# Optimization experiments

Hardware: AMD Instinct MI355X
Metric: run time of the kernel (lower is better)

## Reference

```python
import jax, jax.numpy as jnp
import numpy as np
from jax import lax

D_MODEL = 1024
D_STATE = 16
EXPAND = 2
KERNEL = 4
BATCH = 4
SEQ = 4096
LN_EPS = 1e-5


def _ln(x, w, b):
    m = jnp.mean(x, axis=-1, keepdims=True)
    v = jnp.mean((x - m) ** 2, axis=-1, keepdims=True)
    return (x - m) * lax.rsqrt(v + LN_EPS) * w + b


def setup_inputs() -> dict:
    key = jax.random.key(0)
    ks = jax.random.split(key, 16)
    d, n, e, k = D_MODEL, D_STATE, EXPAND, KERNEL

    def lin(key, fan_in, shape):
        bound = 1.0 / np.sqrt(fan_in)
        return jax.random.uniform(key, shape, jnp.float32, -bound, bound)

    return {
        "x": jax.random.normal(ks[0], (BATCH, SEQ, d), jnp.float32),
        "ln1_w": jnp.ones((d,), jnp.float32),
        "ln1_b": jnp.zeros((d,), jnp.float32),
        "conv_w": lin(ks[1], k, (d, 1, k)),  # depthwise conv, groups=d -> fan_in=k
        "conv_b": lin(ks[2], k, (d,)),
        "lns_w": jnp.ones((d,), jnp.float32),
        "lns_b": jnp.zeros((d,), jnp.float32),
        "in_w": lin(ks[3], d, (d, 2 * d)),
        "in_b": lin(ks[4], d, (2 * d,)),
        "xp_w": lin(ks[5], d, (d, n)),
        "xp_b": lin(ks[6], d, (n,)),
        "A_log": jax.random.normal(ks[7], (n,), jnp.float32),
        "D": jax.random.normal(ks[8], (n, d), jnp.float32),
        "out_w": lin(ks[9], d, (d, d)),
        "out_b": lin(ks[10], d, (d,)),
        "ln2_w": jnp.ones((d,), jnp.float32),
        "ln2_b": jnp.zeros((d,), jnp.float32),
        "mlp_w1": lin(ks[11], d, (d, e * d)),
        "mlp_b1": lin(ks[12], d, (e * d,)),
        "mlp_w2": lin(ks[13], e * d, (e * d, d)),
        "mlp_b2": lin(ks[14], e * d, (d,)),
    }


def reference(x, ln1_w, ln1_b, conv_w, conv_b, lns_w, lns_b, in_w, in_b,
              xp_w, xp_b, A_log, D, out_w, out_b, ln2_w, ln2_b,
              mlp_w1, mlp_b1, mlp_w2, mlp_b2):
    b, s, d = x.shape
    # --- depthwise causal-padded conv branch (truncated to seq_len) ---
    xn = _ln(x, ln1_w, ln1_b)
    xc = jnp.transpose(xn, (0, 2, 1))  # (b, d, s)
    xc = lax.conv_general_dilated(
        xc, conv_w, window_strides=(1,), padding=[(KERNEL - 1, KERNEL - 1)],
        feature_group_count=d, dimension_numbers=("NCH", "OIH", "NCH"))
    xc = xc + conv_b[None, :, None]
    xc = jnp.transpose(xc, (0, 2, 1))[:, :s]  # (b, s, d)
    x = x + xc

    # --- SelectiveScanLayer ---
    residual = x
    xn = _ln(x, lns_w, lns_b)
    xz = xn @ in_w + in_b
    xp, z = jnp.split(xz, 2, axis=-1)
    xp = jax.nn.silu(xp)
    z = jax.nn.sigmoid(z)
    u = xp @ xp_w + xp_b  # (b, s, n)
    decay = jnp.exp(-jnp.exp(A_log))  # exp(A), A = -exp(A_log); (n,)

    u_t = jnp.transpose(u, (1, 0, 2))  # (s, b, n)

    def step(h, u_i):
        h = decay * h + u_i
        return h, h

    _, hs = lax.scan(step, jnp.zeros((b, D_STATE), x.dtype), u_t)  # (s, b, n)
    ys = jnp.einsum("sbn,nd->sbd", hs, D) * jnp.transpose(z, (1, 0, 2))
    ys = ys @ out_w + out_b  # (s, b, d)
    # faithful to original: torch stack gives (1,s,b,d), then .view(b,s,d)
    y = ys.reshape(b, s, d)
    x = residual + y

    # --- MLP (dropout inactive at eval) ---
    h = _ln(x, ln2_w, ln2_b)
    h = jax.nn.gelu(h @ mlp_w1 + mlp_b1, approximate=False)
    h = h @ mlp_w2 + mlp_b2
    return x + h
```

## Files before the change

kernel.cpp:

```cpp
#include <hip/hip_runtime.h>
#include <cstdint>
#include <cstddef>


typedef short bf16x8 __attribute__((ext_vector_type(8)));
typedef float f32x4 __attribute__((ext_vector_type(4)));

#define GLD16(gp, lp)                                                          \
  __builtin_amdgcn_global_load_lds(                                            \
      (__attribute__((address_space(1))) void*)(gp),                           \
      (__attribute__((address_space(3))) void*)(lp), 16, 0, 0)

static __device__ __forceinline__ ushort f2bf(float f) {
  union { float f; uint32_t u; } c; c.f = f;
  uint32_t r = c.u + 0x7FFFu + ((c.u >> 16) & 1u);
  return (ushort)(r >> 16);
}
static __device__ __forceinline__ float bf2f(ushort u) {
  union { uint32_t u; float f; } c; c.u = ((uint32_t)u) << 16;
  return c.f;
}

template <int BF16OUT>
__global__ __launch_bounds__(256) void ln_kernel(
    const float* __restrict__ x, const float* __restrict__ w,
    const float* __restrict__ b, void* __restrict__ out) {
  const int row = blockIdx.x;
  const int tid = threadIdx.x;
  const float4 v = ((const float4*)(x + (size_t)row * 1024))[tid];
  float s  = v.x + v.y + v.z + v.w;
  float s2 = v.x * v.x + v.y * v.y + v.z * v.z + v.w * v.w;
#pragma unroll
  for (int off = 32; off > 0; off >>= 1) {
    s  += __shfl_down(s, off);
    s2 += __shfl_down(s2, off);
  }
  __shared__ float red[8];
  const int wv = tid >> 6, ln = tid & 63;
  if (ln == 0) { red[wv] = s; red[4 + wv] = s2; }
  __syncthreads();
  s  = red[0] + red[1] + red[2] + red[3];
  s2 = red[4] + red[5] + red[6] + red[7];
  const float mean = s * (1.f / 1024.f);
  const float var  = s2 * (1.f / 1024.f) - mean * mean;
  const float rstd = rsqrtf(var + 1e-5f);
  const float4 wv4 = ((const float4*)w)[tid];
  const float4 bv4 = ((const float4*)b)[tid];
  const float o0 = (v.x - mean) * rstd * wv4.x + bv4.x;
  const float o1 = (v.y - mean) * rstd * wv4.y + bv4.y;
  const float o2 = (v.z - mean) * rstd * wv4.z + bv4.z;
  const float o3 = (v.w - mean) * rstd * wv4.w + bv4.w;
  if (BF16OUT) {
    ushort4 o; o.x = f2bf(o0); o.y = f2bf(o1); o.z = f2bf(o2); o.w = f2bf(o3);
    ((ushort4*)((ushort*)out + (size_t)row * 1024))[tid] = o;
  } else {
    float4 o; o.x = o0; o.y = o1; o.z = o2; o.w = o3;
    ((float4*)((float*)out + (size_t)row * 1024))[tid] = o;
  }
}

__global__ __launch_bounds__(256) void lnconv_kernel(
    const float* __restrict__ x, const float* __restrict__ ln1w,
    const float* __restrict__ ln1b, const float* __restrict__ cw,
    const float* __restrict__ cb, const float* __restrict__ lnsw,
    const float* __restrict__ lnsb, float* __restrict__ x1,
    ushort* __restrict__ abuf) {
  const int row = blockIdx.x;
  const int t = row & 4095;
  const int tid = threadIdx.x;
  const int wv = tid >> 6, ln = tid & 63;
  const float4* x4 = (const float4*)x;
  float4 xr[4];
  float s[4], q[4];
#pragma unroll
  for (int j = 0; j < 4; j++) {
    const int tt = t - 3 + j;
    if (tt >= 0)
      xr[j] = x4[(size_t)(row - 3 + j) * 256 + tid];
    else
      xr[j] = make_float4(0.f, 0.f, 0.f, 0.f);
    s[j] = xr[j].x + xr[j].y + xr[j].z + xr[j].w;
    q[j] = xr[j].x * xr[j].x + xr[j].y * xr[j].y + xr[j].z * xr[j].z +
           xr[j].w * xr[j].w;
  }
#pragma unroll
  for (int off = 32; off > 0; off >>= 1) {
#pragma unroll
    for (int j = 0; j < 4; j++) {
      s[j] += __shfl_down(s[j], off);
      q[j] += __shfl_down(q[j], off);
    }
  }
  __shared__ float red[4][8];
  __shared__ float red2[8];
  if (ln == 0) {
#pragma unroll
    for (int j = 0; j < 4; j++) { red[wv][j] = s[j]; red[wv][4 + j] = q[j]; }
  }
  __syncthreads();
  float4 wv4 = ((const float4*)ln1w)[tid];
  float4 bv4 = ((const float4*)ln1b)[tid];
  const int c0 = tid * 4;
  float4 acc = *(const float4*)(cb + c0);
  const float4 w0 = *(const float4*)(cw + (size_t)(c0 + 0) * 4);
  const float4 w1 = *(const float4*)(cw + (size_t)(c0 + 1) * 4);
  const float4 w2 = *(const float4*)(cw + (size_t)(c0 + 2) * 4);
  const float4 w3 = *(const float4*)(cw + (size_t)(c0 + 3) * 4);
#pragma unroll
  for (int j = 0; j < 4; j++) {
    if (t - 3 + j >= 0) {
      const float sm = red[0][j] + red[1][j] + red[2][j] + red[3][j];
      const float sq = red[0][4 + j] + red[1][4 + j] + red[2][4 + j] +
                       red[3][4 + j];
      const float mean = sm * (1.f / 1024.f);
      const float var  = sq * (1.f / 1024.f) - mean * mean;
      const float rstd = rsqrtf(var + 1e-5f);
      const float lx = (xr[j].x - mean) * rstd * wv4.x + bv4.x;
      const float ly = (xr[j].y - mean) * rstd * wv4.y + bv4.y;
      const float lz = (xr[j].z - mean) * rstd * wv4.z + bv4.z;
      const float lw = (xr[j].w - mean) * rstd * wv4.w + bv4.w;
      acc.x += lx * ((const float*)&w0)[j];
      acc.y += ly * ((const float*)&w1)[j];
      acc.z += lz * ((const float*)&w2)[j];
      acc.w += lw * ((const float*)&w3)[j];
    }
  }
  float4 o;
  o.x = xr[3].x + acc.x; o.y = xr[3].y + acc.y;
  o.z = xr[3].z + acc.z; o.w = xr[3].w + acc.w;
  ((float4*)x1)[(size_t)row * 256 + tid] = o;
  float s2 = o.x + o.y + o.z + o.w;
  float q2 = o.x * o.x + o.y * o.y + o.z * o.z + o.w * o.w;
#pragma unroll
  for (int off = 32; off > 0; off >>= 1) {
    s2 += __shfl_down(s2, off);
    q2 += __shfl_down(q2, off);
  }
  if (ln == 0) { red2[wv] = s2; red2[4 + wv] = q2; }
  __syncthreads();
  const float sm = red2[0] + red2[1] + red2[2] + red2[3];
  const float sq = red2[4] + red2[5] + red2[6] + red2[7];
  const float mean = sm * (1.f / 1024.f);
  const float var  = sq * (1.f / 1024.f) - mean * mean;
  const float rstd = rsqrtf(var + 1e-5f);
  wv4 = ((const float4*)lnsw)[tid];
  bv4 = ((const float4*)lnsb)[tid];
  ushort4 a;
  a.x = f2bf((o.x - mean) * rstd * wv4.x + bv4.x);
  a.y = f2bf((o.y - mean) * rstd * wv4.y + bv4.y);
  a.z = f2bf((o.z - mean) * rstd * wv4.z + bv4.z);
  a.w = f2bf((o.w - mean) * rstd * wv4.w + bv4.w);
  ((ushort4*)(abuf + (size_t)row * 1024))[tid] = a;
}

__global__ __launch_bounds__(256) void wt_all_kernel(
    const float* __restrict__ in_w, const float* __restrict__ out_w,
    const float* __restrict__ w1, const float* __restrict__ w2,
    ushort* __restrict__ in_wT, ushort* __restrict__ out_wT,
    ushort* __restrict__ w1T, ushort* __restrict__ w2T) {
  __shared__ float tile[32][33];
  const int idx = blockIdx.x;
  const float* src; ushort* dst; int K, N, n0, k0;
  if (idx < 2048) {
    src = in_w; dst = in_wT; K = 1024; N = 2048;
    n0 = (idx & 63) * 32; k0 = (idx >> 6) * 32;
  } else if (idx < 3072) {
    const int r = idx - 2048;
    src = out_w; dst = out_wT; K = 1024; N = 1024;
    n0 = (r & 31) * 32; k0 = (r >> 5) * 32;
  } else if (idx < 5120) {
    const int r = idx - 3072;
    src = w1; dst = w1T; K = 1024; N = 2048;
    n0 = (r & 63) * 32; k0 = (r >> 6) * 32;
  } else {
    const int r = idx - 5120;
    src = w2; dst = w2T; K = 2048; N = 1024;
    n0 = (r & 31) * 32; k0 = (r >> 5) * 32;
  }
  const int tx = threadIdx.x & 31, ty = threadIdx.x >> 5;
#pragma unroll
  for (int j = 0; j < 32; j += 8)
    tile[ty + j][tx] = src[(size_t)(k0 + ty + j) * N + n0 + tx];
  __syncthreads();
#pragma unroll
  for (int j = 0; j < 32; j += 8)
    dst[(size_t)(n0 + ty + j) * K + k0 + tx] = f2bf(tile[tx][ty + j]);
}

__global__ __launch_bounds__(256) void u_mfma_kernel(
    const ushort* __restrict__ xp, const float* __restrict__ xpw,
    const float* __restrict__ xpb, float* __restrict__ u) {
  __shared__ ushort Ws[16 * 1024];
  __shared__ ushort As[64 * 64];
  const int tid = threadIdx.x;
  const int wave = tid >> 6, lane = tid & 63;
  const int l16 = lane & 15, quad = lane >> 4;
  for (int e = tid; e < 16384; e += 256) {
    const int n = e & 15, k = e >> 4;
    Ws[n * 1024 + (((k >> 3) ^ (n & 7)) << 3) + (k & 7)] =
        f2bf(xpw[(size_t)k * 16 + n]);
  }
  const int bm0 = blockIdx.x * 64;
  const int srow = lane >> 3, sblk = (lane & 7) ^ (srow & 7);
  const ushort* Ag = xp + (size_t)(bm0 + wave * 16 + srow) * 1024 + sblk * 8;
  ushort* Al = &As[wave * 16 * 64];
  const int rsw = l16 & 7;
  f32x4 acc = (f32x4){0.f, 0.f, 0.f, 0.f};
  __syncthreads();
  for (int k0 = 0; k0 < 1024; k0 += 64) {
    GLD16(Ag + k0, Al);
    GLD16(Ag + k0 + (size_t)8 * 1024, Al + 512);
    __syncthreads();
#pragma unroll
    for (int kh = 0; kh < 2; kh++) {
      const bf16x8 aF = *(const bf16x8*)
          &As[(wave * 16 + l16) * 64 + (((kh * 4 + quad) ^ rsw) << 3)];
      const bf16x8 bF = *(const bf16x8*)
          &Ws[l16 * 1024 + ((((k0 >> 3) + kh * 4 + quad) ^ rsw) << 3)];
      acc = __builtin_amdgcn_mfma_f32_16x16x32_bf16(aF, bF, acc, 0, 0, 0);
    }
    __syncthreads();
  }
  const float bv = xpb[l16];
#pragma unroll
  for (int r = 0; r < 4; r++) {
    const int row = bm0 + wave * 16 + quad * 4 + r;
    u[(size_t)row * 16 + l16] = acc[r] + bv;
  }
}

__global__ __launch_bounds__(256) void scan_kernel(
    const float* __restrict__ u, const float* __restrict__ A_log,
    float* __restrict__ hs) {
  const int tid = threadIdx.x;
  const int b = blockIdx.x >> 4;
  const int n = blockIdx.x & 15;
  const float d = expf(-expf(A_log[n]));
  const int t0 = tid * 16;
  const float* up = u + ((size_t)b * 4096) * 16 + n;
  float loc[16];
  float h = 0.f;
#pragma unroll
  for (int i = 0; i < 16; i++) {
    h = d * h + up[(size_t)(t0 + i) * 16];
    loc[i] = h;
  }
  __shared__ float sv[256];
  sv[tid] = h;
  __syncthreads();
  float d16 = d * d; d16 *= d16; d16 *= d16; d16 *= d16;
  float f = d16;
  for (int off = 1; off < 256; off <<= 1) {
    const float add = (tid >= off) ? sv[tid - off] : 0.f;
    __syncthreads();
    sv[tid] += f * add;
    __syncthreads();
    f *= f;
  }
  const float carry = (tid > 0) ? sv[tid - 1] : 0.f;
  float dp = d;
#pragma unroll
  for (int i = 0; i < 16; i++) {
    const float hg = loc[i] + dp * carry;
    dp *= d;
    hs[((size_t)(t0 + i) * 4 + b) * 16 + n] = hg;
  }
}

__global__ __launch_bounds__(256) void g_kernel(
    const float* __restrict__ hs, const float* __restrict__ Dm,
    const ushort* __restrict__ z, ushort* __restrict__ g) {
  __shared__ float hsh[256];
  const int tid = threadIdx.x;
  const int r0 = blockIdx.x * 16;
  hsh[tid] = hs[(size_t)r0 * 16 + tid];
  __syncthreads();
  float4 acc[16];
#pragma unroll
  for (int rr = 0; rr < 16; rr++) acc[rr] = make_float4(0.f, 0.f, 0.f, 0.f);
  const float4* Dv = (const float4*)Dm;
#pragma unroll
  for (int n = 0; n < 16; n++) {
    const float4 dv = Dv[(size_t)n * 256 + tid];
#pragma unroll
    for (int rr = 0; rr < 16; rr++) {
      const float h = hsh[rr * 16 + n];
      acc[rr].x += h * dv.x; acc[rr].y += h * dv.y;
      acc[rr].z += h * dv.z; acc[rr].w += h * dv.w;
    }
  }
#pragma unroll
  for (int rr = 0; rr < 16; rr++) {
    const int r = r0 + rr;
    const int b = r & 3, t = r >> 2;
    const ushort4 zv =
        *(const ushort4*)(z + ((size_t)b * 4096 + t) * 1024 + tid * 4);
    ushort4 o;
    o.x = f2bf(acc[rr].x * bf2f(zv.x)); o.y = f2bf(acc[rr].y * bf2f(zv.y));
    o.z = f2bf(acc[rr].z * bf2f(zv.z)); o.w = f2bf(acc[rr].w * bf2f(zv.w));
    *(ushort4*)(g + (size_t)r * 1024 + tid * 4) = o;
  }
}

template <int EPI>
__global__ __launch_bounds__(512, 2) void gemm_bt(
    const ushort* __restrict__ A, const ushort* __restrict__ Bt,
    const float* __restrict__ bias, int K, void* __restrict__ p0,
    void* __restrict__ p1) {
  __shared__ __align__(16) ushort sm[65536];
  const int tid = threadIdx.x;
  const int wave = tid >> 6, lane = tid & 63;
  const int l16 = lane & 15, quad = lane >> 4;
  const int wm = wave >> 2, wn = wave & 3;

  const int nbx = (int)gridDim.x;
  int tm, tn;
  if ((nbx & 7) == 0) {
    const int lid = (int)blockIdx.y * nbx + (int)blockIdx.x;
    const int ncm = nbx >> 3;
    const int xcd = lid & 7;
    const int j = lid >> 3;
    tm = xcd * ncm + (j % ncm);
    tn = j / ncm;
  } else {
    tm = (int)blockIdx.x; tn = (int)blockIdx.y;
  }
  const int bm0 = tm * 256, bn0 = tn * 256;

  const int srow = lane >> 3;
  const int sblk = (lane & 7) ^ srow;
  const int NT = K >> 6;

  const ushort* Astg = A + (size_t)(bm0 + wave * 8 + srow) * K + sblk * 8;
  const ushort* Bstg = Bt + (size_t)(bn0 + wave * 8 + srow) * K + sblk * 8;

#define SA(i, kt, base)                                                        \
  GLD16(Astg + (size_t)((i) * 64) * K + (kt) * 64,                             \
        &sm[(base) + (i) * 4096 + wave * 512])
#define SB(i, kt, base)                                                        \
  GLD16(Bstg + (size_t)((i) * 64) * K + (kt) * 64,                             \
        &sm[(base) + 16384 + (i) * 4096 + wave * 512])

  const int rsw = l16 & 7;
  const int c80 = (quad ^ rsw) << 3;
  const int c81 = ((4 + quad) ^ rsw) << 3;
  const int aoff = (wm * 128 + l16) * 64;
  const int boff = 16384 + (wn * 64 + l16) * 64;

  f32x4 acc[8][4];
#pragma unroll
  for (int i = 0; i < 8; i++)
#pragma unroll
    for (int j = 0; j < 4; j++) acc[i][j] = (f32x4){0.f, 0.f, 0.f, 0.f};

#pragma unroll
  for (int i = 0; i < 4; i++) { SA(i, 0, 0); SB(i, 0, 0); }
  if (NT > 1) {
#pragma unroll
    for (int i = 0; i < 4; i++) { SA(i, 1, 32768); SB(i, 1, 32768); }
    asm volatile("s_waitcnt vmcnt(8)" ::: "memory");
  } else {
    asm volatile("s_waitcnt vmcnt(0)" ::: "memory");
  }
  __builtin_amdgcn_s_barrier();

  bf16x8 af[4][2], b01[2][2], b23[2][2];

  for (int t = 0; t < NT; ++t) {
    const int cb = (t & 1) << 15;
#pragma unroll
    for (int i = 0; i < 4; i++) {
      af[i][0] = *(const bf16x8*)&sm[cb + aoff + i * 1024 + c80];
      af[i][1] = *(const bf16x8*)&sm[cb + aoff + i * 1024 + c81];
    }
#pragma unroll
    for (int j = 0; j < 2; j++) {
      b01[j][0] = *(const bf16x8*)&sm[cb + boff + j * 1024 + c80];
      b01[j][1] = *(const bf16x8*)&sm[cb + boff + j * 1024 + c81];
    }
    __builtin_amdgcn_s_barrier();
    asm volatile("s_waitcnt lgkmcnt(0)" ::: "memory");
    __builtin_amdgcn_sched_barrier(0);
    __builtin_amdgcn_s_setprio(1);
#pragma unroll
    for (int i = 0; i < 4; i++)
#pragma unroll
      for (int j = 0; j < 2; j++) {
        acc[i][j] = __builtin_amdgcn_mfma_f32_16x16x32_bf16(
            b01[j][0], af[i][0], acc[i][j], 0, 0, 0);
        acc[i][j] = __builtin_amdgcn_mfma_f32_16x16x32_bf16(
            b01[j][1], af[i][1], acc[i][j], 0, 0, 0);
      }
    __builtin_amdgcn_s_setprio(0);
    __builtin_amdgcn_s_barrier();
#pragma unroll
    for (int j = 0; j < 2; j++) {
      b23[j][0] = *(const bf16x8*)&sm[cb + boff + (2 + j) * 1024 + c80];
      b23[j][1] = *(const bf16x8*)&sm[cb + boff + (2 + j) * 1024 + c81];
    }
    __builtin_amdgcn_s_barrier();
    asm volatile("s_waitcnt lgkmcnt(0)" ::: "memory");
    __builtin_amdgcn_sched_barrier(0);
    __builtin_amdgcn_s_setprio(1);
#pragma unroll
    for (int i = 0; i < 4; i++)
#pragma unroll
      for (int j = 0; j < 2; j++) {
        acc[i][2 + j] = __builtin_amdgcn_mfma_f32_16x16x32_bf16(
            b23[j][0], af[i][0], acc[i][2 + j], 0, 0, 0);
        acc[i][2 + j] = __builtin_amdgcn_mfma_f32_16x16x32_bf16(
            b23[j][1], af[i][1], acc[i][2 + j], 0, 0, 0);
      }
    __builtin_amdgcn_s_setprio(0);
    __builtin_amdgcn_s_barrier();
#pragma unroll
    for (int i = 0; i < 4; i++) {
      af[i][0] = *(const bf16x8*)&sm[cb + aoff + (4 + i) * 1024 + c80];
      af[i][1] = *(const bf16x8*)&sm[cb + aoff + (4 + i) * 1024 + c81];
    }
    __builtin_amdgcn_s_barrier();
    asm volatile("s_waitcnt lgkmcnt(0)" ::: "memory");
    __builtin_amdgcn_sched_barrier(0);
    __builtin_amdgcn_s_setprio(1);
#pragma unroll
    for (int i = 0; i < 4; i++)
#pragma unroll
      for (int j = 0; j < 2; j++) {
        acc[4 + i][j] = __builtin_amdgcn_mfma_f32_16x16x32_bf16(
            b01[j][0], af[i][0], acc[4 + i][j], 0, 0, 0);
        acc[4 + i][j] = __builtin_amdgcn_mfma_f32_16x16x32_bf16(
            b01[j][1], af[i][1], acc[4 + i][j], 0, 0, 0);
      }
    __builtin_amdgcn_s_setprio(0);
    __builtin_amdgcn_s_barrier();
    if (t + 2 < NT) {
#pragma unroll
      for (int i = 0; i < 4; i++) { SA(i, t + 2, cb); SB(i, t + 2, cb); }
    }
    __builtin_amdgcn_s_setprio(1);
#pragma unroll
    for (int i = 0; i < 4; i++)
#pragma unroll
      for (int j = 0; j < 2; j++) {
        acc[4 + i][2 + j] = __builtin_amdgcn_mfma_f32_16x16x32_bf16(
            b23[j][0], af[i][0], acc[4 + i][2 + j], 0, 0, 0);
        acc[4 + i][2 + j] = __builtin_amdgcn_mfma_f32_16x16x32_bf16(
            b23[j][1], af[i][1], acc[4 + i][2 + j], 0, 0, 0);
      }
    __builtin_amdgcn_s_setprio(0);
    if (t + 2 < NT) {
      asm volatile("s_waitcnt vmcnt(8)" ::: "memory");
    } else {
      asm volatile("s_waitcnt vmcnt(0)" ::: "memory");
    }
    __builtin_amdgcn_s_barrier();
  }
#undef SA
#undef SB

#pragma unroll
  for (int i = 0; i < 8; i++) {
    const size_t row = (size_t)(bm0 + wm * 128 + i * 16 + l16);
#pragma unroll
    for (int j = 0; j < 4; j++) {
      const int c = bn0 + wn * 64 + j * 16 + quad * 4;
      const float4 bv = *(const float4*)(bias + c);
      const float v0 = acc[i][j][0] + bv.x;
      const float v1 = acc[i][j][1] + bv.y;
      const float v2 = acc[i][j][2] + bv.z;
      const float v3 = acc[i][j][3] + bv.w;
      if (EPI == 0) {
        ushort4 o;
        if (c < 1024) {
          o.x = f2bf(v0 / (1.f + __expf(-v0)));
          o.y = f2bf(v1 / (1.f + __expf(-v1)));
          o.z = f2bf(v2 / (1.f + __expf(-v2)));
          o.w = f2bf(v3 / (1.f + __expf(-v3)));
          *(ushort4*)((ushort*)p0 + row * 1024 + c) = o;
        } else {
          o.x = f2bf(1.f / (1.f + __expf(-v0)));
          o.y = f2bf(1.f / (1.f + __expf(-v1)));
          o.z = f2bf(1.f / (1.f + __expf(-v2)));
          o.w = f2bf(1.f / (1.f + __expf(-v3)));
          *(ushort4*)((ushort*)p1 + row * 1024 + (c - 1024)) = o;
        }
      } else if (EPI == 1) {
        float4* io = (float4*)((float*)p0 + row * 1024 + c);
        float4 t4 = *io;
        t4.x += v0; t4.y += v1; t4.z += v2; t4.w += v3;
        *io = t4;
      } else if (EPI == 2) {
        ushort4 o;
        o.x = f2bf(0.5f * v0 * (1.f + erff(v0 * 0.70710678118654752f)));
        o.y = f2bf(0.5f * v1 * (1.f + erff(v1 * 0.70710678118654752f)));
        o.z = f2bf(0.5f * v2 * (1.f + erff(v2 * 0.70710678118654752f)));
        o.w = f2bf(0.5f * v3 * (1.f + erff(v3 * 0.70710678118654752f)));
        *(ushort4*)((ushort*)p0 + row * 2048 + c) = o;
      } else {
        const float4 pv = *(const float4*)((const float*)p1 + row * 1024 + c);
        float4 t4;
        t4.x = pv.x + v0; t4.y = pv.y + v1;
        t4.z = pv.z + v2; t4.w = pv.w + v3;
        *(float4*)((float*)p0 + row * 1024 + c) = t4;
      }
    }
  }
}

extern "C" void kernel_launch(void* const* d_in, const int* in_sizes, int n_in,
                              void* d_out, int out_size, void* d_ws,
                              size_t ws_size, hipStream_t stream) {
  const float* x      = (const float*)d_in[0];
  const float* ln1_w  = (const float*)d_in[1];
  const float* ln1_b  = (const float*)d_in[2];
  const float* conv_w = (const float*)d_in[3];
  const float* conv_b = (const float*)d_in[4];
  const float* lns_w  = (const float*)d_in[5];
  const float* lns_b  = (const float*)d_in[6];
  const float* in_w   = (const float*)d_in[7];
  const float* in_b   = (const float*)d_in[8];
  const float* xp_w   = (const float*)d_in[9];
  const float* xp_b   = (const float*)d_in[10];
  const float* A_log  = (const float*)d_in[11];
  const float* Dm     = (const float*)d_in[12];
  const float* out_w  = (const float*)d_in[13];
  const float* out_b  = (const float*)d_in[14];
  const float* ln2_w  = (const float*)d_in[15];
  const float* ln2_b  = (const float*)d_in[16];
  const float* mlp_w1 = (const float*)d_in[17];
  const float* mlp_b1 = (const float*)d_in[18];
  const float* mlp_w2 = (const float*)d_in[19];
  const float* mlp_b2 = (const float*)d_in[20];

  char* wsp = (char*)d_ws;
  size_t off = 0;
  auto alloc = [&](size_t bytes) {
    void* p = wsp + off;
    off += (bytes + 255) & ~(size_t)255;
    return p;
  };
  float*  x1    = (float*)alloc(67108864);
  ushort* abuf  = (ushort*)alloc(67108864);
  ushort* gbuf  = abuf + 16777216;
  ushort* xpb   = (ushort*)alloc(33554432);
  ushort* zb    = (ushort*)alloc(67108864);
  ushort* h1b   = (ushort*)zb;
  float*  ub    = (float*)alloc(1048576);
  float*  hsb   = (float*)alloc(1048576);
  ushort* in_wT = (ushort*)alloc(4194304);
  ushort* out_wT= (ushort*)alloc(2097152);
  ushort* w1T   = (ushort*)alloc(4194304);
  ushort* w2T   = (ushort*)alloc(4194304);

  wt_all_kernel<<<7168, 256, 0, stream>>>(in_w, out_w, mlp_w1, mlp_w2,
                                          in_wT, out_wT, w1T, w2T);
  lnconv_kernel<<<16384, 256, 0, stream>>>(x, ln1_w, ln1_b, conv_w, conv_b,
                                           lns_w, lns_b, x1, abuf);
  gemm_bt<0><<<dim3(64, 8), 512, 0, stream>>>(abuf, in_wT, in_b, 1024,
                                              xpb, zb);
  u_mfma_kernel<<<256, 256, 0, stream>>>(xpb, xp_w, xp_b, ub);
  scan_kernel<<<64, 256, 0, stream>>>(ub, A_log, hsb);
  g_kernel<<<1024, 256, 0, stream>>>(hsb, Dm, zb, gbuf);
  gemm_bt<1><<<dim3(64, 4), 512, 0, stream>>>(gbuf, out_wT, out_b, 1024,
                                              x1, nullptr);
  ln_kernel<1><<<16384, 256, 0, stream>>>(x1, ln2_w, ln2_b, xpb);
  gemm_bt<2><<<dim3(64, 8), 512, 0, stream>>>(xpb, w1T, mlp_b1, 1024,
                                              h1b, nullptr);
  gemm_bt<3><<<dim3(64, 4), 512, 0, stream>>>(h1b, w2T, mlp_b2, 2048,
                                              d_out, x1);
}
```

Before: 636.9 us.

## Precompute LN1 row stats once and use one wavefront per row in LN kernels

A new rowstats kernel computes mean and rstd for each input row once and stores them. The fused LN+conv kernel then reads those stats for the three previous rows instead of recomputing four row reductions per output row. Both LN kernels now map one wavefront to one row, so the reduction needs only shuffles and no shared memory or barriers. The cost is an extra kernel launch and a second full read of x. The conv kernel still reads four neighbouring x rows, which are mostly expected to hit in cache.

```diff
diff --git a/kernel.cpp b/kernel.cpp
--- a/kernel.cpp
+++ b/kernel.cpp
@@ -21,136 +21,144 @@
   return c.f;
 }
 
+__global__ __launch_bounds__(256) void rowstats_kernel(
+    const float* __restrict__ x, float2* __restrict__ stats) {
+  const int row = blockIdx.x * 4 + (threadIdx.x >> 6);
+  const int lane = threadIdx.x & 63;
+  const float4* xr = (const float4*)(x + (size_t)row * 1024);
+  float s = 0.f, q = 0.f;
+#pragma unroll
+  for (int i = 0; i < 4; i++) {
+    const float4 v = xr[lane + i * 64];
+    s += v.x + v.y + v.z + v.w;
+    q += v.x * v.x + v.y * v.y + v.z * v.z + v.w * v.w;
+  }
+#pragma unroll
+  for (int off = 32; off > 0; off >>= 1) {
+    s += __shfl_down(s, off);
+    q += __shfl_down(q, off);
+  }
+  if (lane == 0) {
+    const float mean = s * (1.f / 1024.f);
+    const float var  = q * (1.f / 1024.f) - mean * mean;
+    stats[row] = make_float2(mean, rsqrtf(var + 1e-5f));
+  }
+}
+
+__global__ __launch_bounds__(256) void lnconv_kernel(
+    const float* __restrict__ x, const float2* __restrict__ stats,
+    const float* __restrict__ ln1w, const float* __restrict__ ln1b,
+    const float* __restrict__ cw, const float* __restrict__ cb,
+    const float* __restrict__ lnsw, const float* __restrict__ lnsb,
+    float* __restrict__ x1, ushort* __restrict__ abuf) {
+  const int row = blockIdx.x * 4 + (threadIdx.x >> 6);
+  const int t = row & 4095;
+  const int lane = threadIdx.x & 63;
+  const float4* x4 = (const float4*)x;
+
+  float2 st[4];
+#pragma unroll
+  for (int j = 0; j < 4; j++)
+    st[j] = (t - 3 + j >= 0) ? stats[row - 3 + j] : make_float2(0.f, 0.f);
+
+  float4 o[4];
+  float s = 0.f, q = 0.f;
+#pragma unroll
+  for (int i = 0; i < 4; i++) {
+    const int f4 = lane + i * 64;
+    const int c0 = f4 * 4;
+    float4 acc = *(const float4*)(cb + c0);
+    const float4 w0 = *(const float4*)(cw + (size_t)(c0 + 0) * 4);
+    const float4 w1 = *(const float4*)(cw + (size_t)(c0 + 1) * 4);
+    const float4 w2 = *(const float4*)(cw + (size_t)(c0 + 2) * 4);
+    const float4 w3 = *(const float4*)(cw + (size_t)(c0 + 3) * 4);
+    const float4 wv4 = ((const float4*)ln1w)[f4];
+    const float4 bv4 = ((const float4*)ln1b)[f4];
+    float4 xm = make_float4(0.f, 0.f, 0.f, 0.f);
+#pragma unroll
+    for (int j = 0; j < 4; j++) {
+      if (t - 3 + j >= 0) {
+        const float4 xv = x4[(size_t)(row - 3 + j) * 256 + f4];
+        if (j == 3) xm = xv;
+        const float mean = st[j].x, rstd = st[j].y;
+        const float lx = (xv.x - mean) * rstd * wv4.x + bv4.x;
+        const float ly = (xv.y - mean) * rstd * wv4.y + bv4.y;
+        const float lz = (xv.z - mean) * rstd * wv4.z + bv4.z;
+        const float lw = (xv.w - mean) * rstd * wv4.w + bv4.w;
+        acc.x += lx * ((const float*)&w0)[j];
+        acc.y += ly * ((const float*)&w1)[j];
+        acc.z += lz * ((const float*)&w2)[j];
+        acc.w += lw * ((const float*)&w3)[j];
+      }
+    }
+    o[i].x = xm.x + acc.x; o[i].y = xm.y + acc.y;
+    o[i].z = xm.z + acc.z; o[i].w = xm.w + acc.w;
+    ((float4*)x1)[(size_t)row * 256 + f4] = o[i];
+    s += o[i].x + o[i].y + o[i].z + o[i].w;
+    q += o[i].x * o[i].x + o[i].y * o[i].y + o[i].z * o[i].z + o[i].w * o[i].w;
+  }
+#pragma unroll
+  for (int off = 1; off < 64; off <<= 1) {
+    s += __shfl_xor(s, off);
+    q += __shfl_xor(q, off);
+  }
+  const float mean = s * (1.f / 1024.f);
+  const float var  = q * (1.f / 1024.f) - mean * mean;
+  const float rstd = rsqrtf(var + 1e-5f);
+#pragma unroll
+  for (int i = 0; i < 4; i++) {
+    const int f4 = lane + i * 64;
+    const float4 wv4 = ((const float4*)lnsw)[f4];
+    const float4 bv4 = ((const float4*)lnsb)[f4];
+    ushort4 a;
+    a.x = f2bf((o[i].x - mean) * rstd * wv4.x + bv4.x);
+    a.y = f2bf((o[i].y - mean) * rstd * wv4.y + bv4.y);
+    a.z = f2bf((o[i].z - mean) * rstd * wv4.z + bv4.z);
+    a.w = f2bf((o[i].w - mean) * rstd * wv4.w + bv4.w);
+    ((ushort4*)(abuf + (size_t)row * 1024))[f4] = a;
+  }
+}
+
 template <int BF16OUT>
 __global__ __launch_bounds__(256) void ln_kernel(
     const float* __restrict__ x, const float* __restrict__ w,
     const float* __restrict__ b, void* __restrict__ out) {
-  const int row = blockIdx.x;
-  const int tid = threadIdx.x;
-  const float4 v = ((const float4*)(x + (size_t)row * 1024))[tid];
-  float s  = v.x + v.y + v.z + v.w;
-  float s2 = v.x * v.x + v.y * v.y + v.z * v.z + v.w * v.w;
-#pragma unroll
-  for (int off = 32; off > 0; off >>= 1) {
-    s  += __shfl_down(s, off);
-    s2 += __shfl_down(s2, off);
-  }
-  __shared__ float red[8];
-  const int wv = tid >> 6, ln = tid & 63;
-  if (ln == 0) { red[wv] = s; red[4 + wv] = s2; }
-  __syncthreads();
-  s  = red[0] + red[1] + red[2] + red[3];
-  s2 = red[4] + red[5] + red[6] + red[7];
+  const int row = blockIdx.x * 4 + (threadIdx.x >> 6);
+  const int lane = threadIdx.x & 63;
+  const float4* xr = (const float4*)(x + (size_t)row * 1024);
+  float4 v[4];
+  float s = 0.f, q = 0.f;
+#pragma unroll
+  for (int i = 0; i < 4; i++) {
+    v[i] = xr[lane + i * 64];
+    s += v[i].x + v[i].y + v[i].z + v[i].w;
+    q += v[i].x * v[i].x + v[i].y * v[i].y + v[i].z * v[i].z + v[i].w * v[i].w;
+  }
+#pragma unroll
+  for (int off = 1; off < 64; off <<= 1) {
+    s += __shfl_xor(s, off);
+    q += __shfl_xor(q, off);
+  }
   const float mean = s * (1.f / 1024.f);
-  const float var  = s2 * (1.f / 1024.f) - mean * mean;
+  const float var  = q * (1.f / 1024.f) - mean * mean;
   const float rstd = rsqrtf(var + 1e-5f);
-  const float4 wv4 = ((const float4*)w)[tid];
-  const float4 bv4 = ((const float4*)b)[tid];
-  const float o0 = (v.x - mean) * rstd * wv4.x + bv4.x;
-  const float o1 = (v.y - mean) * rstd * wv4.y + bv4.y;
-  const float o2 = (v.z - mean) * rstd * wv4.z + bv4.z;
-  const float o3 = (v.w - mean) * rstd * wv4.w + bv4.w;
-  if (BF16OUT) {
-    ushort4 o; o.x = f2bf(o0); o.y = f2bf(o1); o.z = f2bf(o2); o.w = f2bf(o3);
-    ((ushort4*)((ushort*)out + (size_t)row * 1024))[tid] = o;
-  } else {
-    float4 o; o.x = o0; o.y = o1; o.z = o2; o.w = o3;
-    ((float4*)((float*)out + (size_t)row * 1024))[tid] = o;
-  }
-}
-
-__global__ __launch_bounds__(256) void lnconv_kernel(
-    const float* __restrict__ x, const float* __restrict__ ln1w,
-    const float* __restrict__ ln1b, const float* __restrict__ cw,
-    const float* __restrict__ cb, const float* __restrict__ lnsw,
-    const float* __restrict__ lnsb, float* __restrict__ x1,
-    ushort* __restrict__ abuf) {
-  const int row = blockIdx.x;
-  const int t = row & 4095;
-  const int tid = threadIdx.x;
-  const int wv = tid >> 6, ln = tid & 63;
-  const float4* x4 = (const float4*)x;
-  float4 xr[4];
-  float s[4], q[4];
-#pragma unroll
-  for (int j = 0; j < 4; j++) {
-    const int tt = t - 3 + j;
-    if (tt >= 0)
-      xr[j] = x4[(size_t)(row - 3 + j) * 256 + tid];
-    else
-      xr[j] = make_float4(0.f, 0.f, 0.f, 0.f);
-    s[j] = xr[j].x + xr[j].y + xr[j].z + xr[j].w;
-    q[j] = xr[j].x * xr[j].x + xr[j].y * xr[j].y + xr[j].z * xr[j].z +
-           xr[j].w * xr[j].w;
-  }
-#pragma unroll
-  for (int off = 32; off > 0; off >>= 1) {
-#pragma unroll
-    for (int j = 0; j < 4; j++) {
-      s[j] += __shfl_down(s[j], off);
-      q[j] += __shfl_down(q[j], off);
-    }
-  }
-  __shared__ float red[4][8];
-  __shared__ float red2[8];
-  if (ln == 0) {
-#pragma unroll
-    for (int j = 0; j < 4; j++) { red[wv][j] = s[j]; red[wv][4 + j] = q[j]; }
-  }
-  __syncthreads();
-  float4 wv4 = ((const float4*)ln1w)[tid];
-  float4 bv4 = ((const float4*)ln1b)[tid];
-  const int c0 = tid * 4;
-  float4 acc = *(const float4*)(cb + c0);
-  const float4 w0 = *(const float4*)(cw + (size_t)(c0 + 0) * 4);
-  const float4 w1 = *(const float4*)(cw + (size_t)(c0 + 1) * 4);
-  const float4 w2 = *(const float4*)(cw + (size_t)(c0 + 2) * 4);
-  const float4 w3 = *(const float4*)(cw + (size_t)(c0 + 3) * 4);
-#pragma unroll
-  for (int j = 0; j < 4; j++) {
-    if (t - 3 + j >= 0) {
-      const float sm = red[0][j] + red[1][j] + red[2][j] + red[3][j];
-      const float sq = red[0][4 + j] + red[1][4 + j] + red[2][4 + j] +
-                       red[3][4 + j];
-      const float mean = sm * (1.f / 1024.f);
-      const float var  = sq * (1.f / 1024.f) - mean * mean;
-      const float rstd = rsqrtf(var + 1e-5f);
-      const float lx = (xr[j].x - mean) * rstd * wv4.x + bv4.x;
-      const float ly = (xr[j].y - mean) * rstd * wv4.y + bv4.y;
-      const float lz = (xr[j].z - mean) * rstd * wv4.z + bv4.z;
-      const float lw = (xr[j].w - mean) * rstd * wv4.w + bv4.w;
-      acc.x += lx * ((const float*)&w0)[j];
-      acc.y += ly * ((const float*)&w1)[j];
-      acc.z += lz * ((const float*)&w2)[j];
-      acc.w += lw * ((const float*)&w3)[j];
-    }
-  }
-  float4 o;
-  o.x = xr[3].x + acc.x; o.y = xr[3].y + acc.y;
-  o.z = xr[3].z + acc.z; o.w = xr[3].w + acc.w;
-  ((float4*)x1)[(size_t)row * 256 + tid] = o;
-  float s2 = o.x + o.y + o.z + o.w;
-  float q2 = o.x * o.x + o.y * o.y + o.z * o.z + o.w * o.w;
-#pragma unroll
-  for (int off = 32; off > 0; off >>= 1) {
-    s2 += __shfl_down(s2, off);
-    q2 += __shfl_down(q2, off);
-  }
-  if (ln == 0) { red2[wv] = s2; red2[4 + wv] = q2; }
-  __syncthreads();
-  const float sm = red2[0] + red2[1] + red2[2] + red2[3];
-  const float sq = red2[4] + red2[5] + red2[6] + red2[7];
-  const float mean = sm * (1.f / 1024.f);
-  const float var  = sq * (1.f / 1024.f) - mean * mean;
-  const float rstd = rsqrtf(var + 1e-5f);
-  wv4 = ((const float4*)lnsw)[tid];
-  bv4 = ((const float4*)lnsb)[tid];
-  ushort4 a;
-  a.x = f2bf((o.x - mean) * rstd * wv4.x + bv4.x);
-  a.y = f2bf((o.y - mean) * rstd * wv4.y + bv4.y);
-  a.z = f2bf((o.z - mean) * rstd * wv4.z + bv4.z);
-  a.w = f2bf((o.w - mean) * rstd * wv4.w + bv4.w);
-  ((ushort4*)(abuf + (size_t)row * 1024))[tid] = a;
+#pragma unroll
+  for (int i = 0; i < 4; i++) {
+    const int f4 = lane + i * 64;
+    const float4 wv4 = ((const float4*)w)[f4];
+    const float4 bv4 = ((const float4*)b)[f4];
+    const float o0 = (v[i].x - mean) * rstd * wv4.x + bv4.x;
+    const float o1 = (v[i].y - mean) * rstd * wv4.y + bv4.y;
+    const float o2 = (v[i].z - mean) * rstd * wv4.z + bv4.z;
+    const float o3 = (v[i].w - mean) * rstd * wv4.w + bv4.w;
+    if (BF16OUT) {
+      ushort4 o; o.x = f2bf(o0); o.y = f2bf(o1); o.z = f2bf(o2); o.w = f2bf(o3);
+      ((ushort4*)((ushort*)out + (size_t)row * 1024))[f4] = o;
+    } else {
+      float4 o; o.x = o0; o.y = o1; o.z = o2; o.w = o3;
+      ((float4*)((float*)out + (size_t)row * 1024))[f4] = o;
+    }
+  }
 }
 
 __global__ __launch_bounds__(256) void wt_all_kernel(
@@ -547,6 +555,7 @@
   ushort* h1b   = (ushort*)zb;
   float*  ub    = (float*)alloc(1048576);
   float*  hsb   = (float*)alloc(1048576);
+  float2* stb   = (float2*)alloc(131072);
   ushort* in_wT = (ushort*)alloc(4194304);
   ushort* out_wT= (ushort*)alloc(2097152);
   ushort* w1T   = (ushort*)alloc(4194304);
@@ -554,8 +563,9 @@
 
   wt_all_kernel<<<7168, 256, 0, stream>>>(in_w, out_w, mlp_w1, mlp_w2,
                                           in_wT, out_wT, w1T, w2T);
-  lnconv_kernel<<<16384, 256, 0, stream>>>(x, ln1_w, ln1_b, conv_w, conv_b,
-                                           lns_w, lns_b, x1, abuf);
+  rowstats_kernel<<<4096, 256, 0, stream>>>(x, stb);
+  lnconv_kernel<<<4096, 256, 0, stream>>>(x, stb, ln1_w, ln1_b, conv_w,
+                                          conv_b, lns_w, lns_b, x1, abuf);
   gemm_bt<0><<<dim3(64, 8), 512, 0, stream>>>(abuf, in_wT, in_b, 1024,
                                               xpb, zb);
   u_mfma_kernel<<<256, 256, 0, stream>>>(xpb, xp_w, xp_b, ub);
@@ -563,7 +573,7 @@
   g_kernel<<<1024, 256, 0, stream>>>(hsb, Dm, zb, gbuf);
   gemm_bt<1><<<dim3(64, 4), 512, 0, stream>>>(gbuf, out_wT, out_b, 1024,
                                               x1, nullptr);
-  ln_kernel<1><<<16384, 256, 0, stream>>>(x1, ln2_w, ln2_b, xpb);
+  ln_kernel<1><<<4096, 256, 0, stream>>>(x1, ln2_w, ln2_b, xpb);
   gemm_bt<2><<<dim3(64, 8), 512, 0, stream>>>(xpb, w1T, mlp_b1, 1024,
                                               h1b, nullptr);
   gemm_bt<3><<<dim3(64, 4), 512, 0, stream>>>(h1b, w2T, mlp_b2, 2048,
```

New measurement: 638.4 us. No clear change (+0.2%).
